# Kernel optimization log

Measured on AMD Instinct MI355X. Metric: run time of the kernel, lower is better.

The kernel has to match this reference:

```python
import jax, jax.numpy as jnp
import numpy as np

B, N, D = 128, 512, 128   # batch, nodes (= patch_len / time_window_size), feature dim (d_model_patch)
EPS = 1e-5                # torch BatchNorm1d default eps
SLOPE = 0.01              # torch F.leaky_relu default negative_slope
DIAG_INF = 1e8            # eyes_like * 100000000.0 in Dot_Graph_Construction_weights


def mask_matrix(T, decay):
    # Faithful replication of Mask_Matrix: slices i*T:(i+1)*T on a [T,T] array
    # are empty for i >= 1, so the result is all ones; we replicate exactly.
    A = np.ones((T, T), np.float32)
    for i in range(T):
        v = 0
        for r in range(i, T):
            A[i * T:(i + 1) * T, r * T:(r + 1) * T] *= decay ** v
            v += 1
        v = 0
        for r in range(i + 1):
            A[i * T:(i + 1) * T, (i - r) * T:(i - r + 1) * T] *= decay ** v
            v += 1
    return A


def setup_inputs() -> dict:
    key = jax.random.key(0)
    ks = jax.random.split(key, 3)
    s = 1.0 / np.sqrt(D)  # torch Linear default init scale
    return {
        "x": jax.random.normal(ks[0], (B, N, D), jnp.float32),
        "W_map": jax.random.uniform(ks[1], (D, D), jnp.float32, -s, s),
        "b_map": jnp.zeros((D,), jnp.float32),
        "W_theta": jax.random.uniform(ks[2], (D, D), jnp.float32, -s, s),
        "b_theta": jnp.zeros((D,), jnp.float32),
        "gamma_in": jnp.ones((D,), jnp.float32),
        "beta_in": jnp.zeros((D,), jnp.float32),
        "gamma_out": jnp.ones((D,), jnp.float32),
        "beta_out": jnp.zeros((D,), jnp.float32),
        "pre_relation": jnp.asarray(mask_matrix(N, 0.9)),
    }


def leaky_relu(x):
    return jnp.where(x >= 0, x, SLOPE * x)


def batchnorm(x, gamma, beta):
    # x: [B, N, C]; BatchNorm1d over channel C (training-mode batch stats,
    # matching torch transpose -> BN -> transpose pattern).
    mean = x.mean((0, 1))
    var = x.var((0, 1))
    return (x - mean) * jax.lax.rsqrt(var + EPS) * gamma + beta


def reference(x, W_map, b_map, W_theta, b_theta, gamma_in, beta_in,
              gamma_out, beta_out, pre_relation):
    # --- Dot_Graph_Construction_weights ---
    nf = x @ W_map + b_map                         # [B,N,D]
    adj = jnp.einsum('bnd,bmd->bnm', nf, nf)       # [B,N,N]
    eye = jnp.eye(N, dtype=x.dtype)
    adj = leaky_relu(adj - eye * DIAG_INF)
    adj = jax.nn.softmax(adj, axis=-1) + eye
    # --- decay mask (all-ones, computed faithfully) ---
    adj = adj * pre_relation
    # --- input BN ---
    xb = batchnorm(x, gamma_in, beta_in)
    # --- MPNN_mk_v2, k=1 ---
    h = jnp.einsum('bnm,bmd->bnd', adj, xb) @ W_theta + b_theta
    h = batchnorm(h, gamma_out, beta_out)
    return leaky_relu(h)                           # [B,N,D]
```

## Files before the change

### kernel.cpp

```cpp
#include <hip/hip_runtime.h>
#include <hip/hip_bf16.h>

#define B_ 128
#define N_ 512
#define D_ 128
#define M_ (B_ * N_)
#define LDSP 136

typedef unsigned short u16;
typedef short s8v __attribute__((ext_vector_type(8)));
typedef _Float16 h8v __attribute__((ext_vector_type(8)));
typedef __fp16 fp2v __attribute__((ext_vector_type(2)));
typedef float f4v __attribute__((ext_vector_type(4)));
typedef unsigned u4v __attribute__((ext_vector_type(4)));

__device__ __forceinline__ u16 f2h(float f) {
  _Float16 h = (_Float16)f;
  return __builtin_bit_cast(u16, h);
}
__device__ __forceinline__ float h2f(u16 v) {
  return (float)__builtin_bit_cast(_Float16, v);
}
__device__ __forceinline__ unsigned cvtpk_h(float a, float b) {
  fp2v r = __builtin_amdgcn_cvt_pkrtz(a, b);
  return __builtin_bit_cast(unsigned, r);
}
__device__ __forceinline__ u16* swzK(u16* base, int row, int col) {
  return (u16*)((char*)base + row * 256 + ((col * 2) ^ ((row & 15) << 4)));
}
__device__ __forceinline__ u16* swz64(u16* base, int row, int col) {
  return (u16*)((char*)base + row * 128 + ((col * 2) ^ ((row & 7) << 4)));
}
__device__ __forceinline__ int kperm(int c) {
  return (c & 3) + ((c >> 2) & 1) * 16 + ((c >> 3) & 3) * 4 + (c >> 5) * 32;
}
__device__ __forceinline__ void derive_ss(const float* __restrict__ stats,
                                          const float* __restrict__ gamma,
                                          const float* __restrict__ beta,
                                          float* sSS, int t) {
  if (t < 128) {
    float mean = stats[t] * (1.0f / (float)M_);
    float var  = stats[128 + t] * (1.0f / (float)M_) - mean * mean;
    float sc = gamma[t] * rsqrtf(var + 1e-5f);
    sSS[t] = sc;
    sSS[128 + t] = beta[t] - mean * sc;
  }
}

__global__ __launch_bounds__(256) void prologue(const float* __restrict__ Wa,
                                                const float* __restrict__ Wb,
                                                u16* __restrict__ WT1,
                                                u16* __restrict__ WT2,
                                                const float* __restrict__ X,
                                                float* __restrict__ stats) {
  const int t = threadIdx.x;
  const int id = blockIdx.x;
  if (id < 128) {
    const float* W = (id < 64) ? Wa : Wb;
    u16* T = (id < 64) ? WT1 : WT2;
    const int idx = (id & 63) * 256 + t;
    const int k = idx >> 7, j = idx & 127;
    T[j * 128 + k] = f2h(W[idx]);
    return;
  }
  const int g = t & 31;
  const int h = t >> 5;
  const size_t r0 = (size_t)(id - 128) * 256;
  float s[4] = {0.f, 0.f, 0.f, 0.f}, q[4] = {0.f, 0.f, 0.f, 0.f};
  for (int r = h; r < 256; r += 8) {
    float4 v = *(const float4*)&X[(r0 + r) * D_ + g * 4];
    s[0] += v.x; q[0] += v.x * v.x;
    s[1] += v.y; q[1] += v.y * v.y;
    s[2] += v.z; q[2] += v.z * v.z;
    s[3] += v.w; q[3] += v.w * v.w;
  }
  __shared__ float red[256][8];
#pragma unroll
  for (int j = 0; j < 4; ++j) { red[t][j] = s[j]; red[t][4 + j] = q[j]; }
  __syncthreads();
  if (t < 32) {
    float S[4] = {0.f, 0.f, 0.f, 0.f}, Q[4] = {0.f, 0.f, 0.f, 0.f};
    for (int hh = 0; hh < 8; ++hh) {
      const float* p = red[hh * 32 + t];
#pragma unroll
      for (int j = 0; j < 4; ++j) { S[j] += p[j]; Q[j] += p[4 + j]; }
    }
#pragma unroll
    for (int j = 0; j < 4; ++j) {
      atomicAdd(&stats[t * 4 + j], S[j]);
      atomicAdd(&stats[128 + t * 4 + j], Q[j]);
    }
  }
}

__global__ __launch_bounds__(256) void xbT_kernel(const float* __restrict__ X,
                                                  const float* __restrict__ stats,
                                                  const float* __restrict__ gamma,
                                                  const float* __restrict__ beta,
                                                  u16* __restrict__ XBT) {
  __shared__ __align__(16) u16 sT[128][LDSP];
  __shared__ float sSS[256];
  const int t = threadIdx.x;
  const int b = blockIdx.x >> 2;
  const int n0 = (blockIdx.x & 3) * 128;
  const size_t xbase = (size_t)b * N_ * D_;
  const size_t tbase = (size_t)b * D_ * N_;
  derive_ss(stats, gamma, beta, sSS, t);
  __syncthreads();
  {
    const int r = t >> 1, c0 = (t & 1) * 64;
#pragma unroll
    for (int i = 0; i < 16; ++i) {
      const int c = c0 + i * 4;
      float4 v = *(const float4*)&X[xbase + (size_t)(n0 + r) * D_ + c];
      sT[c + 0][r] = f2h(v.x * sSS[c + 0] + sSS[128 + c + 0]);
      sT[c + 1][r] = f2h(v.y * sSS[c + 1] + sSS[128 + c + 1]);
      sT[c + 2][r] = f2h(v.z * sSS[c + 2] + sSS[128 + c + 2]);
      sT[c + 3][r] = f2h(v.w * sSS[c + 3] + sSS[128 + c + 3]);
    }
  }
  __syncthreads();
  {
    const int d = t >> 1, nc = (t & 1) * 64;
#pragma unroll
    for (int i = 0; i < 8; ++i) {
      u16 o[8];
#pragma unroll
      for (int e = 0; e < 8; ++e) {
        const int L = nc + i * 8 + e;
        o[e] = sT[d][kperm(L & 63) + (L & 64)];
      }
      *(s8v*)&XBT[tbase + (size_t)d * N_ + n0 + nc + i * 8] = *(const s8v*)o;
    }
  }
}

__global__ __launch_bounds__(256, 2) void gemm1(const float* __restrict__ A,
                                                const u16* __restrict__ WT,
                                                const float* __restrict__ bias,
                                                u16* __restrict__ C) {
  __shared__ __align__(16) u16 sW[128][LDSP];
  const int t = threadIdx.x;
  const int wv = t >> 6, ln = t & 63, l16 = ln & 15, kg = ln >> 4;
  const size_t row0 = (size_t)blockIdx.x * 128;

#pragma unroll
  for (int i = 0; i < 8; ++i) {
    int o = t * 8 + i * 2048;
    *(s8v*)&sW[o >> 7][o & 127] = *(const s8v*)&WT[o];
  }

  h8v af[2][4];
#pragma unroll
  for (int rf = 0; rf < 2; ++rf) {
    const size_t row = row0 + wv * 32 + rf * 16 + l16;
#pragma unroll
    for (int kt = 0; kt < 4; ++kt) {
      const float* p = &A[row * D_ + kt * 32 + kg * 8];
      float4 v0 = *(const float4*)p;
      float4 v1 = *(const float4*)(p + 4);
      u16 hh[8];
      hh[0] = f2h(v0.x); hh[1] = f2h(v0.y); hh[2] = f2h(v0.z); hh[3] = f2h(v0.w);
      hh[4] = f2h(v1.x); hh[5] = f2h(v1.y); hh[6] = f2h(v1.z); hh[7] = f2h(v1.w);
      af[rf][kt] = *(const h8v*)hh;
    }
  }
  __syncthreads();

  f4v acc[2][8];
#pragma unroll
  for (int rf = 0; rf < 2; ++rf)
#pragma unroll
    for (int jf = 0; jf < 8; ++jf) acc[rf][jf] = f4v{0.f, 0.f, 0.f, 0.f};

#pragma unroll
  for (int kt = 0; kt < 4; ++kt) {
    const int k0 = kt * 32 + kg * 8;
#pragma unroll
    for (int jf = 0; jf < 8; ++jf) {
      h8v bw = *(const h8v*)&sW[jf * 16 + l16][k0];
      acc[0][jf] = __builtin_amdgcn_mfma_f32_16x16x32_f16(af[0][kt], bw, acc[0][jf], 0, 0, 0);
      acc[1][jf] = __builtin_amdgcn_mfma_f32_16x16x32_f16(af[1][kt], bw, acc[1][jf], 0, 0, 0);
    }
  }

#pragma unroll
  for (int rf = 0; rf < 2; ++rf) {
#pragma unroll
    for (int reg = 0; reg < 4; ++reg) {
      const int row = wv * 32 + rf * 16 + kg * 4 + reg;
#pragma unroll
      for (int jf = 0; jf < 8; ++jf) {
        const int col = jf * 16 + l16;
        C[(row0 + row) * D_ + col] = f2h(acc[rf][jf][reg] + bias[col]);
      }
    }
  }
}

__global__ __launch_bounds__(256, 2) void gemm2(const u16* __restrict__ A,
                                                const u16* __restrict__ WT,
                                                const float* __restrict__ bias,
                                                u16* __restrict__ C,
                                                float* __restrict__ stats) {
  __shared__ __align__(16) u16 sW[128][LDSP];
  __shared__ float sSum[128], sSq[128];
  const int t = threadIdx.x;
  const int wv = t >> 6, ln = t & 63, l16 = ln & 15, kg = ln >> 4;
  const size_t row0 = (size_t)blockIdx.x * 128;

  if (t < 128) { sSum[t] = 0.f; sSq[t] = 0.f; }
#pragma unroll
  for (int i = 0; i < 8; ++i) {
    int o = t * 8 + i * 2048;
    *(s8v*)&sW[o >> 7][o & 127] = *(const s8v*)&WT[o];
  }

  h8v a[2][4];
#pragma unroll
  for (int rf = 0; rf < 2; ++rf) {
    const size_t row = row0 + wv * 32 + rf * 16 + l16;
#pragma unroll
    for (int kt = 0; kt < 4; ++kt)
      a[rf][kt] = *(const h8v*)&A[row * D_ + kt * 32 + kg * 8];
  }
  __syncthreads();

  f4v acc[2][8];
#pragma unroll
  for (int rf = 0; rf < 2; ++rf)
#pragma unroll
    for (int jf = 0; jf < 8; ++jf) acc[rf][jf] = f4v{0.f, 0.f, 0.f, 0.f};

#pragma unroll
  for (int kt = 0; kt < 4; ++kt) {
    const int k0 = kt * 32 + kg * 8;
#pragma unroll
    for (int jf = 0; jf < 8; ++jf) {
      h8v bw = *(const h8v*)&sW[jf * 16 + l16][k0];
      acc[0][jf] = __builtin_amdgcn_mfma_f32_16x16x32_f16(a[0][kt], bw, acc[0][jf], 0, 0, 0);
      acc[1][jf] = __builtin_amdgcn_mfma_f32_16x16x32_f16(a[1][kt], bw, acc[1][jf], 0, 0, 0);
    }
  }

  float cs[8], cq[8];
#pragma unroll
  for (int jf = 0; jf < 8; ++jf) { cs[jf] = 0.f; cq[jf] = 0.f; }
#pragma unroll
  for (int rf = 0; rf < 2; ++rf) {
#pragma unroll
    for (int reg = 0; reg < 4; ++reg) {
      const int row = wv * 32 + rf * 16 + kg * 4 + reg;
#pragma unroll
      for (int jf = 0; jf < 8; ++jf) {
        const int col = jf * 16 + l16;
        u16 hb = f2h(acc[rf][jf][reg] + bias[col]);
        C[(row0 + row) * D_ + col] = hb;
        float vr = h2f(hb);
        cs[jf] += vr;
        cq[jf] += vr * vr;
      }
    }
  }
#pragma unroll
  for (int jf = 0; jf < 8; ++jf) {
    cs[jf] += __shfl_xor(cs[jf], 16); cq[jf] += __shfl_xor(cq[jf], 16);
    cs[jf] += __shfl_xor(cs[jf], 32); cq[jf] += __shfl_xor(cq[jf], 32);
  }
  if (kg == 0) {
#pragma unroll
    for (int jf = 0; jf < 8; ++jf) {
      atomicAdd(&sSum[jf * 16 + l16], cs[jf]);
      atomicAdd(&sSq[jf * 16 + l16], cq[jf]);
    }
  }
  __syncthreads();
  if (t < 128) {
    atomicAdd(&stats[t], sSum[t]);
    atomicAdd(&stats[128 + t], sSq[t]);
  }
}

__global__ __launch_bounds__(512, 4) void attn_kernel(const u16* __restrict__ NF,
                                                      const u16* __restrict__ XBT,
                                                      const float* __restrict__ X,
                                                      const float* __restrict__ stats,
                                                      const float* __restrict__ gamma,
                                                      const float* __restrict__ beta,
                                                      u16* __restrict__ ATT) {
  __shared__ __align__(16) u16 pool[17408];
  __shared__ float sSS[256];
  u16* sK  = pool;
  u16* sVT = pool + 8192;
  const int t = threadIdx.x;
  const int wv = t >> 6, ln = t & 63, l16 = ln & 15, kg = ln >> 4;
  const int id = blockIdx.x;
  const int b = (id & 7) + (id >> 5) * 8;
  const int r0 = ((id >> 3) & 3) * 128;
  const size_t base  = (size_t)b * N_ * D_;
  const size_t baseT = (size_t)b * D_ * N_;

  derive_ss(stats, gamma, beta, sSS, t);

  h8v qf[4];
  {
    const size_t qoff = base + (size_t)(r0 + wv * 16 + l16) * D_ + kg * 8;
#pragma unroll
    for (int kt = 0; kt < 4; ++kt)
      qf[kt] = *(const h8v*)&NF[qoff + kt * 32];
  }

  const int kr = t >> 3, kc = (t & 7) * 16;
  const int vd = t >> 2, vc = (t & 3) * 16;
  const u16* gK = &NF[base + (size_t)kr * D_ + kc];
  const u16* gV = &XBT[baseT + (size_t)vd * N_ + vc];
  s8v rh0 = *(const s8v*)gK, rh1 = *(const s8v*)(gK + 8);
  s8v rv0 = *(const s8v*)gV, rv1 = *(const s8v*)(gV + 8);

  float m = -3e38f, l = 0.f;
  f4v accO[8];
#pragma unroll
  for (int df = 0; df < 8; ++df) accO[df] = f4v{0.f, 0.f, 0.f, 0.f};

  const int qg = r0 + wv * 16 + l16;
  const int qtile = qg & ~63;

  for (int j0 = 0; j0 < N_; j0 += 64) {
    *(s8v*)swzK(sK, kr, kc)       = rh0;
    *(s8v*)swzK(sK, kr, kc + 8)   = rh1;
    *(s8v*)swz64(sVT, vd, vc)     = rv0;
    *(s8v*)swz64(sVT, vd, vc + 8) = rv1;
    __syncthreads();
    if (j0 + 64 < N_) {
      const int jn = j0 + 64;
      rh0 = *(const s8v*)(gK + (size_t)jn * D_);
      rh1 = *(const s8v*)(gK + (size_t)jn * D_ + 8);
      rv0 = *(const s8v*)(gV + jn);
      rv1 = *(const s8v*)(gV + jn + 8);
    }

    f4v accS[4];
#pragma unroll
    for (int jf = 0; jf < 4; ++jf) accS[jf] = f4v{0.f, 0.f, 0.f, 0.f};
    __builtin_amdgcn_s_setprio(1);
#pragma unroll
    for (int kt = 0; kt < 4; ++kt) {
      const int k0 = kt * 32 + kg * 8;
#pragma unroll
      for (int jf = 0; jf < 4; ++jf) {
        h8v k_ = *(const h8v*)swzK(sK, jf * 16 + l16, k0);
        accS[jf] = __builtin_amdgcn_mfma_f32_16x16x32_f16(k_, qf[kt], accS[jf], 0, 0, 0);
      }
    }
    __builtin_amdgcn_s_setprio(0);

    float mx = -3e38f;
    if (j0 == qtile) {
#pragma unroll
      for (int jf = 0; jf < 4; ++jf) {
#pragma unroll
        for (int reg = 0; reg < 4; ++reg) {
          const int kk = j0 + jf * 16 + kg * 4 + reg;
          float sv = accS[jf][reg];
          if (kk == qg) sv -= 1e8f;
          sv = (sv >= 0.f) ? sv : 0.01f * sv;
          accS[jf][reg] = sv;
          mx = fmaxf(mx, sv);
        }
      }
    } else {
#pragma unroll
      for (int jf = 0; jf < 4; ++jf) {
#pragma unroll
        for (int reg = 0; reg < 4; ++reg) {
          float sv = accS[jf][reg];
          sv = (sv >= 0.f) ? sv : 0.01f * sv;
          accS[jf][reg] = sv;
          mx = fmaxf(mx, sv);
        }
      }
    }
    mx = fmaxf(mx, __shfl_xor(mx, 16));
    mx = fmaxf(mx, __shfl_xor(mx, 32));
    const bool resc = !__all(mx - m <= 8.0f);
    const float mnew = resc ? fmaxf(m, mx) : m;
    float rs = 0.f;
#pragma unroll
    for (int jf = 0; jf < 4; ++jf) {
#pragma unroll
      for (int reg = 0; reg < 4; ++reg) {
        const float p = __expf(accS[jf][reg] - mnew);
        accS[jf][reg] = p;
        rs += p;
      }
    }
    rs += __shfl_xor(rs, 16);
    rs += __shfl_xor(rs, 32);
    if (resc) {
      const float scl = __expf(m - mnew);
      l = l * scl + rs;
      m = mnew;
#pragma unroll
      for (int df = 0; df < 8; ++df) accO[df] = accO[df] * scl;
    } else {
      l += rs;
    }

    u4v w0, w1;
    w0[0] = cvtpk_h(accS[0][0], accS[0][1]);
    w0[1] = cvtpk_h(accS[0][2], accS[0][3]);
    w0[2] = cvtpk_h(accS[1][0], accS[1][1]);
    w0[3] = cvtpk_h(accS[1][2], accS[1][3]);
    w1[0] = cvtpk_h(accS[2][0], accS[2][1]);
    w1[1] = cvtpk_h(accS[2][2], accS[2][3]);
    w1[2] = cvtpk_h(accS[3][0], accS[3][1]);
    w1[3] = cvtpk_h(accS[3][2], accS[3][3]);
    h8v pb0, pb1;
    __builtin_memcpy(&pb0, &w0, 16);
    __builtin_memcpy(&pb1, &w1, 16);

    __builtin_amdgcn_s_setprio(1);
#pragma unroll
    for (int kt2 = 0; kt2 < 2; ++kt2) {
      const int k0 = kt2 * 32 + kg * 8;
      const h8v pb = kt2 ? pb1 : pb0;
#pragma unroll
      for (int df = 0; df < 8; ++df) {
        h8v av = *(const h8v*)swz64(sVT, df * 16 + l16, k0);
        accO[df] = __builtin_amdgcn_mfma_f32_16x16x32_f16(av, pb, accO[df], 0, 0, 0);
      }
    }
    __builtin_amdgcn_s_setprio(0);
    __syncthreads();
  }

  const float inv = 1.0f / l;
  u16* sOut = pool;
#pragma unroll
  for (int df = 0; df < 8; ++df) {
#pragma unroll
    for (int reg = 0; reg < 4; ++reg) {
      const int d = df * 16 + kg * 4 + reg;
      sOut[d * 136 + wv * 16 + l16] = f2h(accO[df][reg] * inv);
    }
  }
  __syncthreads();
  {
    const int q = t >> 2, c0 = (t & 3) * 32;
    const size_t orow = base + (size_t)(r0 + q) * D_;
#pragma unroll
    for (int i = 0; i < 4; ++i) {
      u16 o[8];
#pragma unroll
      for (int e = 0; e < 8; ++e) {
        const int d = c0 + i * 8 + e;
        const float ov = h2f(sOut[d * 136 + q]);
        const float xb = X[orow + d] * sSS[d] + sSS[128 + d];
        o[e] = f2h(ov + xb);
      }
      *(s8v*)&ATT[orow + c0 + i * 8] = *(const s8v*)o;
    }
  }
}

__global__ __launch_bounds__(256) void affine_out(const u16* __restrict__ H,
                                                  const float* __restrict__ stats,
                                                  const float* __restrict__ gamma,
                                                  const float* __restrict__ beta,
                                                  float* __restrict__ Y) {
  __shared__ float sSS[256];
  const int t = threadIdx.x;
  derive_ss(stats, gamma, beta, sSS, t);
  __syncthreads();
  const size_t idx = (size_t)blockIdx.x * 256 + t;
  const int c0 = (int)(idx & 15) * 8;
  s8v v = *(const s8v*)&H[idx * 8];
  float o[8];
#pragma unroll
  for (int e = 0; e < 8; ++e) {
    float x = h2f((u16)v[e]);
    float y = x * sSS[c0 + e] + sSS[128 + c0 + e];
    o[e] = (y >= 0.f) ? y : 0.01f * y;
  }
  *(float4*)&Y[idx * 8]     = make_float4(o[0], o[1], o[2], o[3]);
  *(float4*)&Y[idx * 8 + 4] = make_float4(o[4], o[5], o[6], o[7]);
}

extern "C" void kernel_launch(void* const* d_in, const int* in_sizes, int n_in,
                              void* d_out, int out_size, void* d_ws, size_t ws_size,
                              hipStream_t stream) {
  const float* x         = (const float*)d_in[0];
  const float* W_map     = (const float*)d_in[1];
  const float* b_map     = (const float*)d_in[2];
  const float* W_theta   = (const float*)d_in[3];
  const float* b_theta   = (const float*)d_in[4];
  const float* gamma_in  = (const float*)d_in[5];
  const float* beta_in   = (const float*)d_in[6];
  const float* gamma_out = (const float*)d_in[7];
  const float* beta_out  = (const float*)d_in[8];
  float* out = (float*)d_out;

  char* ws = (char*)d_ws;
  float* stats_x = (float*)ws;
  float* stats_h = (float*)(ws + 1024);
  u16* WT1 = (u16*)(ws + 2048);
  u16* WT2 = WT1 + 128 * 128;
  const size_t BUF = (size_t)M_ * D_;
  u16* nf = WT2 + 128 * 128;

  u16* xbT  = (u16*)d_out;
  u16* attO = (u16*)d_out + BUF;

  (void)hipMemsetAsync(ws, 0, 2048, stream);

  prologue<<<384, 256, 0, stream>>>(W_map, W_theta, WT1, WT2, x, stats_x);
  gemm1<<<512, 256, 0, stream>>>(x, WT1, b_map, nf);
  xbT_kernel<<<512, 256, 0, stream>>>(x, stats_x, gamma_in, beta_in, xbT);
  attn_kernel<<<512, 512, 0, stream>>>(nf, xbT, x, stats_x, gamma_in, beta_in, attO);
  gemm2<<<512, 256, 0, stream>>>(attO, WT2, b_theta, nf, stats_h);
  affine_out<<<4096, 256, 0, stream>>>(nf, stats_h, gamma_out, beta_out, out);
}
```

Baseline: 143.9 us.

## Double-buffer K/V shared tiles in attention and split prologue stats over more blocks

The attention kernel now keeps two LDS buffers for K and V tiles. It writes the prefetched next tile into the spare buffer after the MFMA work, so each iteration needs one barrier instead of a store-then-barrier at the top. The prologue's column-statistics pass now uses blocks of 64 rows instead of 256, tripling the grid to raise parallelism. The costs are twice the LDS per block, which may lower occupancy at 512 threads with launch bounds of 4, and four times as many atomic adds in the stats reduction.

```diff
diff --git a/kernel.cpp b/kernel.cpp
--- a/kernel.cpp
+++ b/kernel.cpp
@@ -65,9 +65,10 @@
   }
   const int g = t & 31;
   const int h = t >> 5;
-  const size_t r0 = (size_t)(id - 128) * 256;
+  const size_t r0 = (size_t)(id - 128) * 64;
   float s[4] = {0.f, 0.f, 0.f, 0.f}, q[4] = {0.f, 0.f, 0.f, 0.f};
-  for (int r = h; r < 256; r += 8) {
+#pragma unroll
+  for (int r = h; r < 64; r += 8) {
     float4 v = *(const float4*)&X[(r0 + r) * D_ + g * 4];
     s[0] += v.x; q[0] += v.x * v.x;
     s[1] += v.y; q[1] += v.y * v.y;
@@ -288,10 +289,12 @@
                                                       const float* __restrict__ gamma,
                                                       const float* __restrict__ beta,
                                                       u16* __restrict__ ATT) {
-  __shared__ __align__(16) u16 pool[17408];
+  __shared__ __align__(16) u16 pool[32768];
   __shared__ float sSS[256];
-  u16* sK  = pool;
-  u16* sVT = pool + 8192;
+  u16* sK0 = pool;
+  u16* sK1 = pool + 8192;
+  u16* sV0 = pool + 16384;
+  u16* sV1 = pool + 24576;
   const int t = threadIdx.x;
   const int wv = t >> 6, ln = t & 63, l16 = ln & 15, kg = ln >> 4;
   const int id = blockIdx.x;
@@ -325,13 +328,16 @@
   const int qg = r0 + wv * 16 + l16;
   const int qtile = qg & ~63;
 
-  for (int j0 = 0; j0 < N_; j0 += 64) {
-    *(s8v*)swzK(sK, kr, kc)       = rh0;
-    *(s8v*)swzK(sK, kr, kc + 8)   = rh1;
-    *(s8v*)swz64(sVT, vd, vc)     = rv0;
-    *(s8v*)swz64(sVT, vd, vc + 8) = rv1;
-    __syncthreads();
-    if (j0 + 64 < N_) {
+  *(s8v*)swzK(sK0, kr, kc)       = rh0;
+  *(s8v*)swzK(sK0, kr, kc + 8)   = rh1;
+  *(s8v*)swz64(sV0, vd, vc)      = rv0;
+  *(s8v*)swz64(sV0, vd, vc + 8)  = rv1;
+  __syncthreads();
+
+  int j0 = 0;
+  auto body = [&](u16* sKc, u16* sVc, u16* sKn, u16* sVn) {
+    const bool hasnext = (j0 + 64) < N_;
+    if (hasnext) {
       const int jn = j0 + 64;
       rh0 = *(const s8v*)(gK + (size_t)jn * D_);
       rh1 = *(const s8v*)(gK + (size_t)jn * D_ + 8);
@@ -348,7 +354,7 @@
       const int k0 = kt * 32 + kg * 8;
 #pragma unroll
       for (int jf = 0; jf < 4; ++jf) {
-        h8v k_ = *(const h8v*)swzK(sK, jf * 16 + l16, k0);
+        h8v k_ = *(const h8v*)swzK(sKc, jf * 16 + l16, k0);
         accS[jf] = __builtin_amdgcn_mfma_f32_16x16x32_f16(k_, qf[kt], accS[jf], 0, 0, 0);
       }
     }
@@ -426,12 +432,26 @@
       const h8v pb = kt2 ? pb1 : pb0;
 #pragma unroll
       for (int df = 0; df < 8; ++df) {
-        h8v av = *(const h8v*)swz64(sVT, df * 16 + l16, k0);
+        h8v av = *(const h8v*)swz64(sVc, df * 16 + l16, k0);
         accO[df] = __builtin_amdgcn_mfma_f32_16x16x32_f16(av, pb, accO[df], 0, 0, 0);
       }
     }
     __builtin_amdgcn_s_setprio(0);
+
+    if (hasnext) {
+      *(s8v*)swzK(sKn, kr, kc)       = rh0;
+      *(s8v*)swzK(sKn, kr, kc + 8)   = rh1;
+      *(s8v*)swz64(sVn, vd, vc)      = rv0;
+      *(s8v*)swz64(sVn, vd, vc + 8)  = rv1;
+    }
     __syncthreads();
+    j0 += 64;
+  };
+
+#pragma unroll 1
+  for (int it = 0; it < 4; ++it) {
+    body(sK0, sV0, sK1, sV1);
+    body(sK1, sV1, sK0, sV0);
   }
 
   const float inv = 1.0f / l;
@@ -513,7 +533,7 @@
 
   (void)hipMemsetAsync(ws, 0, 2048, stream);
 
-  prologue<<<384, 256, 0, stream>>>(W_map, W_theta, WT1, WT2, x, stats_x);
+  prologue<<<1152, 256, 0, stream>>>(W_map, W_theta, WT1, WT2, x, stats_x);
   gemm1<<<512, 256, 0, stream>>>(x, WT1, b_map, nf);
   xbT_kernel<<<512, 256, 0, stream>>>(x, stats_x, gamma_in, beta_in, xbT);
   attn_kernel<<<512, 512, 0, stream>>>(nf, xbT, x, stats_x, gamma_in, beta_in, attO);
```

Result: slower. 212.3 us (+47.5%).
